# Kernel tuning notes

Measured on AMD Instinct MI355X. Metric: run time of the kernel, lower is better.

The kernel has to match this reference:

```python
import jax, jax.numpy as jnp
import numpy as np

N_NODES = 10000
W_DIM = 512
N_EDGES = 200000


def setup_inputs() -> dict:
    key = jax.random.key(0)
    k1, k2, k3 = jax.random.split(key, 3)
    z_drug = jax.random.normal(k1, (N_NODES, W_DIM), dtype=jnp.float32)
    # glorot-style init for the bilinear weight
    glorot_std = jnp.sqrt(2.0 / (W_DIM + W_DIM)).astype(jnp.float32)
    weight = jax.random.normal(k2, (W_DIM, W_DIM), dtype=jnp.float32) * glorot_std
    batch_edges = jax.random.randint(k3, (2, N_EDGES), 0, N_NODES, dtype=jnp.int64)
    return {"z_drug": z_drug, "weight": weight, "batch_edges": batch_edges}


def reference(z_drug, weight, batch_edges):
    # edge_type == 'drug_drug': both endpoints come from the drug table.
    row_embed = z_drug[batch_edges[0]]  # [E, d]
    col_embed = z_drug[batch_edges[1]]  # [E, d]
    # score_e = row_e @ W @ col_e  == diag((Z1 W) Z2^T) without the N x N blowup
    score = jnp.einsum('ed,df,ef->e', row_embed, weight, col_embed)
    return jax.nn.sigmoid(score)  # is_sigmoid=True default
```

## Files before the change

kernel.cpp:

```cpp
#include <hip/hip_runtime.h>
#include <math.h>

#define DIM     512
#define NNODES  10000
#define NEDGES  200000
#define MPAD    10048
#define NMB     157

using short8  = __attribute__((ext_vector_type(8))) short;
using floatx4 = __attribute__((ext_vector_type(4))) float;
using half8   = __attribute__((ext_vector_type(8))) _Float16;

#define PREP_ZBLK 2512
__global__ __launch_bounds__(256) void prep(const float* __restrict__ Z,
                                            const float* __restrict__ W,
                                            _Float16* __restrict__ Zh16,
                                            _Float16* __restrict__ Wh16t,
                                            int* __restrict__ counts) {
    const int b = blockIdx.x;
    const int t = threadIdx.x;

    if (b < 40) {
        int i = b * 256 + t;
        if (i < NNODES) counts[i] = 0;
    }

    if (b < PREP_ZBLK) {
        const int idx8 = (b * 256 + t) * 8;
        const int m = idx8 >> 9;
        float x[8];
        if (m < NNODES) {
            float4 v0 = *(const float4*)(Z + idx8);
            float4 v1 = *(const float4*)(Z + idx8 + 4);
            x[0]=v0.x; x[1]=v0.y; x[2]=v0.z; x[3]=v0.w;
            x[4]=v1.x; x[5]=v1.y; x[6]=v1.z; x[7]=v1.w;
        } else {
            #pragma unroll
            for (int j = 0; j < 8; ++j) x[j] = 0.f;
        }
        half8 h;
        #pragma unroll
        for (int j = 0; j < 8; ++j) h[j] = (_Float16)x[j];
        *(half8*)(Zh16 + idx8) = h;
    } else {
        __shared__ float tile[64][65];
        const int wb = b - PREP_ZBLK;
        const int kb = (wb >> 3) * 64;
        const int nb = (wb & 7) * 64;
        const int kk = t >> 2;
        const int ch = t & 3;

        const float* src = W + (size_t)(kb + kk) * DIM + nb + ch * 16;
        #pragma unroll
        for (int q = 0; q < 4; ++q) {
            float4 v = *(const float4*)(src + q * 4);
            tile[kk][ch * 16 + q * 4 + 0] = v.x;
            tile[kk][ch * 16 + q * 4 + 1] = v.y;
            tile[kk][ch * 16 + q * 4 + 2] = v.z;
            tile[kk][ch * 16 + q * 4 + 3] = v.w;
        }
        __syncthreads();

        const int nn = kk;
        half8 h0, h1;
        #pragma unroll
        for (int i = 0; i < 8; ++i) h0[i] = (_Float16)tile[ch * 16 + i][nn];
        #pragma unroll
        for (int i = 0; i < 8; ++i) h1[i] = (_Float16)tile[ch * 16 + 8 + i][nn];
        _Float16* d = Wh16t + (size_t)(nb + nn) * DIM + kb + ch * 16;
        *(half8*)(d)     = h0;
        *(half8*)(d + 8) = h1;
    }
}

__global__ __launch_bounds__(256) void gemm_f16(const _Float16* __restrict__ Zh16,
                                                const _Float16* __restrict__ Wh16t,
                                                _Float16* __restrict__ ZWh) {
    __shared__ _Float16 Abuf[2][64 * 32];
    __shared__ _Float16 Bbuf[2][128 * 32];

    const int t     = threadIdx.x;
    const int bid   = blockIdx.x;
    const int n_idx = bid & 3;
    const int m0    = (bid >> 2) * 64;
    const int n0    = n_idx * 128;

    const int l  = t & 63;
    const int w  = t >> 6;
    const int wn = w * 32;
    const int lm = l & 15;
    const int lq = l >> 4;
    const unsigned wbase = (unsigned)(t & 192);

    floatx4 acc[4][2] = {};

    const int arow = t >> 2;
    const int ach  = t & 3;

    auto stage = [&](int buf, int k0) {
        {
            const _Float16* s = Zh16 + (size_t)(m0 + arow) * DIM + k0 + ach * 8;
            __builtin_amdgcn_global_load_lds(
                (const __attribute__((address_space(1))) void*)s,
                (__attribute__((address_space(3))) void*)&Abuf[buf][wbase * 8], 16, 0, 0);
        }
        #pragma unroll
        for (int p = 0; p < 2; ++p) {
            const int sidx = p * 256 + t;
            const int row  = sidx >> 2;
            const int ch   = sidx & 3;
            const _Float16* s = Wh16t + (size_t)(n0 + row) * DIM + k0 + ch * 8;
            __builtin_amdgcn_global_load_lds(
                (const __attribute__((address_space(1))) void*)s,
                (__attribute__((address_space(3))) void*)&Bbuf[buf][(p * 256 + wbase) * 8], 16, 0, 0);
        }
    };

    stage(0, 0);
    __syncthreads();

    for (int s = 0; s < 16; ++s) {
        const int buf = s & 1;
        if (s < 15) stage(buf ^ 1, (s + 1) * 32);

        half8 aF[4], bF[2];
        #pragma unroll
        for (int i = 0; i < 4; ++i)
            aF[i] = *(const half8*)&Abuf[buf][(16 * i + lm) * 32 + lq * 8];
        #pragma unroll
        for (int j = 0; j < 2; ++j)
            bF[j] = *(const half8*)&Bbuf[buf][(wn + 16 * j + lm) * 32 + lq * 8];

        #pragma unroll
        for (int i = 0; i < 4; ++i)
            #pragma unroll
            for (int j = 0; j < 2; ++j)
                acc[i][j] = __builtin_amdgcn_mfma_f32_16x16x32_f16(aF[i], bF[j], acc[i][j], 0, 0, 0);

        __syncthreads();
    }

    #pragma unroll
    for (int i = 0; i < 4; ++i)
        #pragma unroll
        for (int j = 0; j < 2; ++j)
            #pragma unroll
            for (int r = 0; r < 4; ++r) {
                const int gm = m0 + 16 * i + lq * 4 + r;
                const int gn = n0 + wn + 16 * j + lm;
                if (gm < NNODES)
                    ZWh[(size_t)gm * DIM + gn] = (_Float16)acc[i][j][r];
            }
}

__global__ void hist_rows(const int* __restrict__ eidx, int* __restrict__ counts) {
    int e = blockIdx.x * blockDim.x + threadIdx.x;
    if (e < NEDGES) atomicAdd(&counts[eidx[e]], 1);
}

__global__ __launch_bounds__(1024) void scan_counts(const int* __restrict__ counts,
                                                    int* __restrict__ offs,
                                                    int* __restrict__ cursor) {
    __shared__ int wsum[16];
    __shared__ int woff[17];
    const int t    = threadIdx.x;
    const int lane = t & 63;
    const int wv   = t >> 6;

    int local[10];
    int s = 0;
    if (t < 1000) {
        #pragma unroll
        for (int j = 0; j < 10; ++j) {
            local[j] = counts[t * 10 + j];
            s += local[j];
        }
    }
    int v = s;
    #pragma unroll
    for (int off = 1; off < 64; off <<= 1) {
        int u = __shfl_up(v, off, 64);
        if (lane >= off) v += u;
    }
    if (lane == 63) wsum[wv] = v;
    __syncthreads();
    if (t == 0) {
        int r = 0;
        #pragma unroll
        for (int i = 0; i < 16; ++i) { woff[i] = r; r += wsum[i]; }
        woff[16] = r;
    }
    __syncthreads();
    if (t < 1000) {
        int run = woff[wv] + (v - s);
        #pragma unroll
        for (int j = 0; j < 10; ++j) {
            offs[t * 10 + j]   = run;
            cursor[t * 10 + j] = run;
            run += local[j];
        }
    }
    if (t == 0) offs[NNODES] = woff[16];
}

__global__ void scatter_edges(const int* __restrict__ eidx,
                              int* __restrict__ cursor,
                              unsigned* __restrict__ keys) {
    int e = blockIdx.x * blockDim.x + threadIdx.x;
    if (e < NEDGES) {
        int r = eidx[e];
        int c = eidx[NEDGES + e];
        int pos = atomicAdd(&cursor[r], 1);
        keys[pos] = ((unsigned)c << 18) | (unsigned)e;
    }
}

__global__ __launch_bounds__(64) void edge_score_h(const _Float16* __restrict__ ZWh,
                                                   const _Float16* __restrict__ Zh,
                                                   const unsigned* __restrict__ keys,
                                                   const int* __restrict__ offs,
                                                   float* __restrict__ out) {
    const int r = blockIdx.x;
    const int start = offs[r];
    const int end   = offs[r + 1];
    if (start == end) return;

    const int lane = threadIdx.x;
    half8 hr = *(const half8*)(ZWh + (size_t)r * DIM + lane * 8);
    float a[8];
    #pragma unroll
    for (int j = 0; j < 8; ++j) a[j] = (float)hr[j];

    int i = start;
    for (; i + 3 < end; i += 4) {
        unsigned k0 = keys[i], k1 = keys[i + 1], k2 = keys[i + 2], k3 = keys[i + 3];
        half8 h0 = *(const half8*)(Zh + (size_t)(k0 >> 18) * DIM + lane * 8);
        half8 h1 = *(const half8*)(Zh + (size_t)(k1 >> 18) * DIM + lane * 8);
        half8 h2 = *(const half8*)(Zh + (size_t)(k2 >> 18) * DIM + lane * 8);
        half8 h3 = *(const half8*)(Zh + (size_t)(k3 >> 18) * DIM + lane * 8);

        float s0 = a[0] * (float)h0[0], s1 = a[0] * (float)h1[0];
        float s2 = a[0] * (float)h2[0], s3 = a[0] * (float)h3[0];
        #pragma unroll
        for (int j = 1; j < 8; ++j) {
            s0 = fmaf(a[j], (float)h0[j], s0);
            s1 = fmaf(a[j], (float)h1[j], s1);
            s2 = fmaf(a[j], (float)h2[j], s2);
            s3 = fmaf(a[j], (float)h3[j], s3);
        }
        #pragma unroll
        for (int off = 32; off > 0; off >>= 1) {
            s0 += __shfl_xor(s0, off, 64);
            s1 += __shfl_xor(s1, off, 64);
            s2 += __shfl_xor(s2, off, 64);
            s3 += __shfl_xor(s3, off, 64);
        }
        if (lane == 0) {
            out[k0 & 0x3FFFFu] = 1.0f / (1.0f + expf(-s0));
            out[k1 & 0x3FFFFu] = 1.0f / (1.0f + expf(-s1));
            out[k2 & 0x3FFFFu] = 1.0f / (1.0f + expf(-s2));
            out[k3 & 0x3FFFFu] = 1.0f / (1.0f + expf(-s3));
        }
    }
    for (; i < end; ++i) {
        unsigned k = keys[i];
        half8 h = *(const half8*)(Zh + (size_t)(k >> 18) * DIM + lane * 8);
        float s = a[0] * (float)h[0];
        #pragma unroll
        for (int j = 1; j < 8; ++j)
            s = fmaf(a[j], (float)h[j], s);
        #pragma unroll
        for (int off = 32; off > 0; off >>= 1)
            s += __shfl_xor(s, off, 64);
        if (lane == 0)
            out[k & 0x3FFFFu] = 1.0f / (1.0f + expf(-s));
    }
}

#define GTM 128
#define GTN 64
#define GTK 16
#define LDA 132
#define LDB 68

__global__ __launch_bounds__(256) void gemm_zw(const float* __restrict__ A,
                                               const float* __restrict__ B,
                                               float* __restrict__ C) {
    __shared__ float As[GTK * LDA];
    __shared__ float Bs[GTK * LDB];

    const int t  = threadIdx.x;
    const int m0 = blockIdx.x * GTM;
    const int n0 = blockIdx.y * GTN;
    const int tx = t & 15;
    const int ty = t >> 4;

    float acc[8][4] = {};

    for (int k0 = 0; k0 < DIM; k0 += GTK) {
        #pragma unroll
        for (int p = 0; p < 2; ++p) {
            int f  = t + p * 256;
            int mm = f >> 2;
            int kq = f & 3;
            int m  = m0 + mm;
            float4 v = make_float4(0.f, 0.f, 0.f, 0.f);
            if (m < NNODES)
                v = *(const float4*)(A + (size_t)m * DIM + k0 + kq * 4);
            As[(kq * 4 + 0) * LDA + mm] = v.x;
            As[(kq * 4 + 1) * LDA + mm] = v.y;
            As[(kq * 4 + 2) * LDA + mm] = v.z;
            As[(kq * 4 + 3) * LDA + mm] = v.w;
        }
        {
            int kb = t >> 4, n4 = t & 15;
            *(float4*)&Bs[kb * LDB + n4 * 4] =
                *(const float4*)(B + (size_t)(k0 + kb) * DIM + n0 + n4 * 4);
        }
        __syncthreads();

        #pragma unroll
        for (int kk = 0; kk < GTK; ++kk) {
            float4 a0 = *(const float4*)&As[kk * LDA + ty * 8];
            float4 a1 = *(const float4*)&As[kk * LDA + ty * 8 + 4];
            float4 b  = *(const float4*)&Bs[kk * LDB + tx * 4];
            float av[8] = {a0.x, a0.y, a0.z, a0.w, a1.x, a1.y, a1.z, a1.w};
            float bv[4] = {b.x, b.y, b.z, b.w};
            #pragma unroll
            for (int i = 0; i < 8; ++i)
                #pragma unroll
                for (int j = 0; j < 4; ++j)
                    acc[i][j] = fmaf(av[i], bv[j], acc[i][j]);
        }
        __syncthreads();
    }

    #pragma unroll
    for (int i = 0; i < 8; ++i) {
        int m = m0 + ty * 8 + i;
        if (m < NNODES)
            *(float4*)(C + (size_t)m * DIM + n0 + tx * 4) =
                make_float4(acc[i][0], acc[i][1], acc[i][2], acc[i][3]);
    }
}

__global__ __launch_bounds__(256) void edge_score(const float* __restrict__ ZW,
                                                  const float* __restrict__ Z,
                                                  const int* __restrict__ eidx,
                                                  float* __restrict__ out) {
    const int e    = blockIdx.x * 4 + (threadIdx.x >> 6);
    const int lane = threadIdx.x & 63;

    const int r = eidx[e];
    const int c = eidx[NEDGES + e];

    const float4* pr = (const float4*)(ZW + (size_t)r * DIM);
    const float4* pc = (const float4*)(Z  + (size_t)c * DIM);

    float4 a0 = pr[lane * 2 + 0];
    float4 a1 = pr[lane * 2 + 1];
    float4 b0 = pc[lane * 2 + 0];
    float4 b1 = pc[lane * 2 + 1];

    float s = a0.x * b0.x;
    s = fmaf(a0.y, b0.y, s);
    s = fmaf(a0.z, b0.z, s);
    s = fmaf(a0.w, b0.w, s);
    s = fmaf(a1.x, b1.x, s);
    s = fmaf(a1.y, b1.y, s);
    s = fmaf(a1.z, b1.z, s);
    s = fmaf(a1.w, b1.w, s);

    #pragma unroll
    for (int off = 32; off > 0; off >>= 1)
        s += __shfl_xor(s, off, 64);

    if (lane == 0)
        out[e] = 1.0f / (1.0f + expf(-s));
}

extern "C" void kernel_launch(void* const* d_in, const int* in_sizes, int n_in,
                              void* d_out, int out_size, void* d_ws, size_t ws_size,
                              hipStream_t stream) {
    const float* Z  = (const float*)d_in[0];
    const float* W  = (const float*)d_in[1];
    const int*   EI = (const int*)d_in[2];
    float* out = (float*)d_out;

    char* p = (char*)d_ws;
    _Float16* ZWh   = (_Float16*)p;  p += (size_t)MPAD * DIM * 2;
    _Float16* Zh16  = (_Float16*)p;  p += (size_t)MPAD * DIM * 2;
    _Float16* Wh16t = (_Float16*)p;  p += (size_t)DIM * DIM * 2;
    int* counts = (int*)p;           p += (size_t)NNODES * 4;
    int* offs   = (int*)p;           p += (size_t)(NNODES + 1) * 4;
    int* cursor = (int*)p;           p += (size_t)NNODES * 4;
    unsigned* keys = (unsigned*)p;   p += (size_t)NEDGES * 4;
    const size_t need_full = (size_t)(p - (char*)d_ws);

    if (ws_size >= need_full) {
        prep<<<PREP_ZBLK + 64, 256, 0, stream>>>(Z, W, Zh16, Wh16t, counts);
        gemm_f16<<<NMB * 4, 256, 0, stream>>>(Zh16, Wh16t, ZWh);
        hist_rows<<<(NEDGES + 255) / 256, 256, 0, stream>>>(EI, counts);
        scan_counts<<<1, 1024, 0, stream>>>(counts, offs, cursor);
        scatter_edges<<<(NEDGES + 255) / 256, 256, 0, stream>>>(EI, cursor, keys);
        edge_score_h<<<NNODES, 64, 0, stream>>>(ZWh, Zh16, keys, offs, out);
    } else {
        float* ZW = (float*)d_ws;
        dim3 g1((NNODES + GTM - 1) / GTM, DIM / GTN);
        gemm_zw<<<g1, 256, 0, stream>>>(Z, W, ZW);
        edge_score<<<NEDGES / 4, 256, 0, stream>>>(ZW, Z, EI, out);
    }
}
```

Measured before the change: 147.8 us.

## Split each wavefront into four 16-lane groups scoring edges with fdot2

The edge scoring kernel now packs four source rows per 256-thread block, and inside each wavefront four 16-lane subgroups each handle one edge. Each lane covers 32 halves with packed fp16 dot2 instructions, so the shuffle reduction needs only four steps. This cuts block count, shuffle overhead and fp16-to-fp32 conversions, and issues wider per-lane loads. The cost is wasted lanes when a row's edge count is not a multiple of four, and fdot2 accumulation rounding that may differ slightly from the previous fp32 FMAs.

New measurement: 145.8 us. Within noise of the previous version (-1.4%).

```diff
diff --git a/kernel.cpp b/kernel.cpp
--- a/kernel.cpp
+++ b/kernel.cpp
@@ -10,6 +10,15 @@
 using short8  = __attribute__((ext_vector_type(8))) short;
 using floatx4 = __attribute__((ext_vector_type(4))) float;
 using half8   = __attribute__((ext_vector_type(8))) _Float16;
+using half2v  = __attribute__((ext_vector_type(2))) _Float16;
+
+__device__ inline float dot2acc(half2v a, half2v b, float c) {
+#if __has_builtin(__builtin_amdgcn_fdot2)
+    return __builtin_amdgcn_fdot2(a, b, c, false);
+#else
+    return fmaf((float)a[0], (float)b[0], fmaf((float)a[1], (float)b[1], c));
+#endif
+}
 
 #define PREP_ZBLK 2512
 __global__ __launch_bounds__(256) void prep(const float* __restrict__ Z,
@@ -215,64 +224,52 @@
     }
 }
 
-__global__ __launch_bounds__(64) void edge_score_h(const _Float16* __restrict__ ZWh,
-                                                   const _Float16* __restrict__ Zh,
-                                                   const unsigned* __restrict__ keys,
-                                                   const int* __restrict__ offs,
-                                                   float* __restrict__ out) {
-    const int r = blockIdx.x;
+__global__ __launch_bounds__(256) void edge_score_q(const _Float16* __restrict__ ZWh,
+                                                    const _Float16* __restrict__ Zh,
+                                                    const unsigned* __restrict__ keys,
+                                                    const int* __restrict__ offs,
+                                                    float* __restrict__ out) {
+    const int r = blockIdx.x * 4 + (threadIdx.x >> 6);
     const int start = offs[r];
     const int end   = offs[r + 1];
     if (start == end) return;
 
-    const int lane = threadIdx.x;
-    half8 hr = *(const half8*)(ZWh + (size_t)r * DIM + lane * 8);
-    float a[8];
-    #pragma unroll
-    for (int j = 0; j < 8; ++j) a[j] = (float)hr[j];
-
-    int i = start;
-    for (; i + 3 < end; i += 4) {
-        unsigned k0 = keys[i], k1 = keys[i + 1], k2 = keys[i + 2], k3 = keys[i + 3];
-        half8 h0 = *(const half8*)(Zh + (size_t)(k0 >> 18) * DIM + lane * 8);
-        half8 h1 = *(const half8*)(Zh + (size_t)(k1 >> 18) * DIM + lane * 8);
-        half8 h2 = *(const half8*)(Zh + (size_t)(k2 >> 18) * DIM + lane * 8);
-        half8 h3 = *(const half8*)(Zh + (size_t)(k3 >> 18) * DIM + lane * 8);
-
-        float s0 = a[0] * (float)h0[0], s1 = a[0] * (float)h1[0];
-        float s2 = a[0] * (float)h2[0], s3 = a[0] * (float)h3[0];
-        #pragma unroll
-        for (int j = 1; j < 8; ++j) {
-            s0 = fmaf(a[j], (float)h0[j], s0);
-            s1 = fmaf(a[j], (float)h1[j], s1);
-            s2 = fmaf(a[j], (float)h2[j], s2);
-            s3 = fmaf(a[j], (float)h3[j], s3);
-        }
-        #pragma unroll
-        for (int off = 32; off > 0; off >>= 1) {
-            s0 += __shfl_xor(s0, off, 64);
-            s1 += __shfl_xor(s1, off, 64);
-            s2 += __shfl_xor(s2, off, 64);
-            s3 += __shfl_xor(s3, off, 64);
-        }
-        if (lane == 0) {
-            out[k0 & 0x3FFFFu] = 1.0f / (1.0f + expf(-s0));
-            out[k1 & 0x3FFFFu] = 1.0f / (1.0f + expf(-s1));
-            out[k2 & 0x3FFFFu] = 1.0f / (1.0f + expf(-s2));
-            out[k3 & 0x3FFFFu] = 1.0f / (1.0f + expf(-s3));
-        }
-    }
-    for (; i < end; ++i) {
-        unsigned k = keys[i];
-        half8 h = *(const half8*)(Zh + (size_t)(k >> 18) * DIM + lane * 8);
-        float s = a[0] * (float)h[0];
-        #pragma unroll
-        for (int j = 1; j < 8; ++j)
-            s = fmaf(a[j], (float)h[j], s);
-        #pragma unroll
-        for (int off = 32; off > 0; off >>= 1)
-            s += __shfl_xor(s, off, 64);
-        if (lane == 0)
+    const int lane = threadIdx.x & 63;
+    const int g    = lane >> 4;
+    const int sl   = lane & 15;
+
+    const _Float16* rp = ZWh + (size_t)r * DIM + sl * 32;
+    half8 ra0 = *(const half8*)(rp);
+    half8 ra1 = *(const half8*)(rp + 8);
+    half8 ra2 = *(const half8*)(rp + 16);
+    half8 ra3 = *(const half8*)(rp + 24);
+
+    for (int i = start; i < end; i += 4) {
+        const int ii = i + g;
+        const unsigned k = keys[ii < end ? ii : (end - 1)];
+        const int c = (int)(k >> 18);
+
+        const _Float16* cp = Zh + (size_t)c * DIM + sl * 32;
+        half8 c0 = *(const half8*)(cp);
+        half8 c1 = *(const half8*)(cp + 8);
+        half8 c2 = *(const half8*)(cp + 16);
+        half8 c3 = *(const half8*)(cp + 24);
+
+        float s = 0.f;
+        #pragma unroll
+        for (int d = 0; d < 4; ++d) {
+            s = dot2acc((half2v){ra0[2*d], ra0[2*d+1]}, (half2v){c0[2*d], c0[2*d+1]}, s);
+            s = dot2acc((half2v){ra1[2*d], ra1[2*d+1]}, (half2v){c1[2*d], c1[2*d+1]}, s);
+            s = dot2acc((half2v){ra2[2*d], ra2[2*d+1]}, (half2v){c2[2*d], c2[2*d+1]}, s);
+            s = dot2acc((half2v){ra3[2*d], ra3[2*d+1]}, (half2v){c3[2*d], c3[2*d+1]}, s);
+        }
+
+        s += __shfl_xor(s, 1, 64);
+        s += __shfl_xor(s, 2, 64);
+        s += __shfl_xor(s, 4, 64);
+        s += __shfl_xor(s, 8, 64);
+
+        if (sl == 0 && ii < end)
             out[k & 0x3FFFFu] = 1.0f / (1.0f + expf(-s));
     }
 }
@@ -403,7 +400,7 @@
         hist_rows<<<(NEDGES + 255) / 256, 256, 0, stream>>>(EI, counts);
         scan_counts<<<1, 1024, 0, stream>>>(counts, offs, cursor);
         scatter_edges<<<(NEDGES + 255) / 256, 256, 0, stream>>>(EI, cursor, keys);
-        edge_score_h<<<NNODES, 64, 0, stream>>>(ZWh, Zh16, keys, offs, out);
+        edge_score_q<<<NNODES / 4, 256, 0, stream>>>(ZWh, Zh16, keys, offs, out);
     } else {
         float* ZW = (float*)d_ws;
         dim3 g1((NNODES + GTM - 1) / GTM, DIM / GTN);
```
